# Kernel optimization log

Measured on AMD Instinct MI355X. Metric: run time of the kernel, lower is better.

## Reference

```python
import jax, jax.numpy as jnp
import numpy as np

HEADS = 16
DIM_HEAD = 64
SCALE = DIM_HEAD ** -0.5


def setup_inputs() -> dict:
    key = jax.random.key(0)
    k1, k2, k3 = jax.random.split(key, 3)
    B, N, C = 2, 2048, 1024
    inner = HEADS * DIM_HEAD  # 1024
    x = jax.random.normal(k1, (B, N, C), dtype=jnp.float32)
    w_qkv = jax.random.normal(k2, (C, 3 * inner), dtype=jnp.float32) * (C ** -0.5)
    w_proj = jax.random.normal(k3, (inner, C), dtype=jnp.float32) * (inner ** -0.5)
    b_proj = jnp.zeros((C,), dtype=jnp.float32)
    return {"x": x, "w_qkv": w_qkv, "w_proj": w_proj, "b_proj": b_proj}


def reference(x, w_qkv, w_proj, b_proj):
    B, N, C = x.shape
    qkv = x @ w_qkv  # [B, N, 3*inner]
    qkv = qkv.reshape(B, N, 3, HEADS, DIM_HEAD)
    qkv = jnp.transpose(qkv, (2, 0, 3, 1, 4))  # [3, B, H, N, D]
    q, k, v = qkv[0], qkv[1], qkv[2]
    q = q * SCALE
    attn = jnp.einsum('bhnd,bhmd->bhnm', q, k)  # [B, H, N, N]
    attn = jax.nn.softmax(attn, axis=-1)
    out = jnp.einsum('bhnm,bhmd->bhnd', attn, v)  # [B, H, N, D]
    out = jnp.transpose(out, (0, 2, 1, 3)).reshape(B, N, HEADS * DIM_HEAD)
    return out @ w_proj + b_proj
```

## Files before the change

### kernel.cpp

```cpp
#include <hip/hip_runtime.h>
#include <hip/hip_bf16.h>
#include <cstdint>
#include <cstddef>

static constexpr int BATCH = 2;
static constexpr int SEQ   = 2048;
static constexpr int CDIM  = 1024;
static constexpr int ROWS  = BATCH * SEQ;
static constexpr int QKVN  = 3 * CDIM;
static constexpr int QKN   = 2 * CDIM;

typedef short bf16x8 __attribute__((ext_vector_type(8)));
typedef short bf16x4 __attribute__((ext_vector_type(4)));
typedef float f32x4  __attribute__((ext_vector_type(4)));

__device__ inline short f2bf(float f) {
    union { float f; unsigned u; } v; v.f = f;
    unsigned u = v.u;
    u += 0x7fffu + ((u >> 16) & 1u);
    return (short)(u >> 16);
}

__device__ inline unsigned pk_bf16(float a, float b) {
#if __has_builtin(__builtin_amdgcn_cvt_pk_bf16_f32)
    auto r = __builtin_amdgcn_cvt_pk_bf16_f32(a, b);
    return __builtin_bit_cast(unsigned, r);
#else
    union { float f; unsigned u; } ua, ub;
    ua.f = a; ub.f = b;
    unsigned xa = ua.u + 0x7fffu + ((ua.u >> 16) & 1u);
    unsigned xb = ub.u + 0x7fffu + ((ub.u >> 16) & 1u);
    return __builtin_amdgcn_perm(xb, xa, 0x07060302);
#endif
}

__device__ inline void glds16(const short* g, short* l) {
    __builtin_amdgcn_global_load_lds(
        (const __attribute__((address_space(1))) void*)g,
        (__attribute__((address_space(3))) void*)l, 16, 0, 0);
}

__device__ inline f32x4 mfma16_bf16(bf16x4 a, bf16x4 b, f32x4 c) {
#if __has_builtin(__builtin_amdgcn_mfma_f32_16x16x16bf16_1k)
    return __builtin_amdgcn_mfma_f32_16x16x16bf16_1k(a, b, c, 0, 0, 0);
#else
    asm("v_mfma_f32_16x16x16_bf16 %0, %1, %2, %0" : "+v"(c) : "v"(a), "v"(b));
    return c;
#endif
}

__device__ inline int swz_src(int lane) {
    return ((lane & 3) ^ ((lane >> 3) & 3)) * 8;
}
__device__ inline int swz_rd(int quad, int l15) {
    return (quad ^ ((l15 >> 1) & 3)) * 8;
}

__global__ __launch_bounds__(256) void prep(const float* __restrict__ x,
                                            const float* __restrict__ wqkv,
                                            const float* __restrict__ wproj,
                                            short* __restrict__ x_bf,
                                            short* __restrict__ wqkvT,
                                            short* __restrict__ wprojT,
                                            float smul) {
    __shared__ float tile[32][33];
    const int bid = blockIdx.x, t = threadIdx.x;
    if (bid < 4096) {
        int i = bid * 256 + t;
        float4 f = ((const float4*)x)[i];
        uint2 o;
        o.x = pk_bf16(f.x, f.y);
        o.y = pk_bf16(f.z, f.w);
        ((uint2*)x_bf)[i] = o;
        return;
    }
    const float* in; short* out; int C, r0, c0; float scale; int srows;
    if (bid < 7168) {
        int b2 = bid - 4096;
        in = wqkv; out = wqkvT; C = QKVN;
        c0 = (b2 % 96) * 32; r0 = (b2 / 96) * 32;
        scale = smul; srows = 1024;
    } else {
        int b3 = bid - 7168;
        in = wproj; out = wprojT; C = CDIM;
        c0 = (b3 & 31) * 32; r0 = (b3 >> 5) * 32;
        scale = 1.0f; srows = 0;
    }
    int tx = t & 31, ty = t >> 5;
    #pragma unroll
    for (int i = 0; i < 4; i++)
        tile[ty + i * 8][tx] = in[(size_t)(r0 + ty + i * 8) * C + c0 + tx];
    __syncthreads();
    #pragma unroll
    for (int i = 0; i < 4; i++) {
        int orow = c0 + ty + i * 8;
        float sc = (orow < srows) ? scale : 1.0f;
        out[(size_t)orow * CDIM + r0 + tx] = f2bf(tile[tx][ty + i * 8] * sc);
    }
}

template<int BF16OUT, int MT>
__device__ __forceinline__ void gemm_core(const short* __restrict__ A,
                                          const short* __restrict__ Bt,
                                          void* __restrict__ C,
                                          const float* __restrict__ bias,
                                          int N, int K, int m0, int n0,
                                          short* As, short* Bs) {
    constexpr int AF = MT / 32;
    constexpr int APAN = MT * 32;
    constexpr int BPAN = 128 * 32;
    const int t = threadIdx.x, wave = t >> 6, lane = t & 63;
    const int l15 = lane & 15, quad = lane >> 4;
    const int wr = wave >> 1, wc = wave & 1;
    const int sg = swz_src(lane);
    const int rsl = swz_rd(quad, l15);

    f32x4 acc[AF][4] = {};

    const short* gA = A  + (size_t)(m0 + wave * (MT / 4) + (lane >> 2)) * K + sg;
    const short* gB = Bt + (size_t)(n0 + wave * 32 + (lane >> 2)) * K + sg;
    short* lA = &As[wave * (MT / 4) * 32];
    short* lB = &Bs[wave * 32 * 32];

    for (int k0 = 0; k0 < K; k0 += 64) {
        glds16(gA + k0,      lA);
        glds16(gA + k0 + 32, lA + APAN);
        if constexpr (MT == 128) {
            glds16(gA + 16 * K + k0,      lA + 512);
            glds16(gA + 16 * K + k0 + 32, lA + APAN + 512);
        }
        glds16(gB + k0,               lB);
        glds16(gB + 16 * K + k0,      lB + 512);
        glds16(gB + k0 + 32,          lB + BPAN);
        glds16(gB + 16 * K + k0 + 32, lB + BPAN + 512);
        __syncthreads();

        #pragma unroll
        for (int st = 0; st < 2; st++) {
            bf16x8 af[AF], bf[4];
            #pragma unroll
            for (int i = 0; i < AF; i++)
                af[i] = *(const bf16x8*)&As[st * APAN + (wr * (MT / 2) + i * 16 + l15) * 32 + rsl];
            #pragma unroll
            for (int j = 0; j < 4; j++)
                bf[j] = *(const bf16x8*)&Bs[st * BPAN + (wc * 64 + j * 16 + l15) * 32 + rsl];
            #pragma unroll
            for (int i = 0; i < AF; i++)
                #pragma unroll
                for (int j = 0; j < 4; j++)
                    acc[i][j] = __builtin_amdgcn_mfma_f32_16x16x32_bf16(af[i], bf[j], acc[i][j], 0, 0, 0);
        }
        __syncthreads();
    }

    #pragma unroll
    for (int i = 0; i < AF; i++) {
        #pragma unroll
        for (int j = 0; j < 4; j++) {
            #pragma unroll
            for (int r = 0; r < 4; r++) {
                int row = m0 + wr * (MT / 2) + i * 16 + quad * 4 + r;
                int col = n0 + wc * 64 + j * 16 + l15;
                float v = acc[i][j][r];
                if (BF16OUT) ((short*)C)[(size_t)row * N + col] = f2bf(v);
                else         ((float*)C)[(size_t)row * N + col] = v + bias[col];
            }
        }
    }
}

__global__ __launch_bounds__(256) void gemm_qk_v(const short* __restrict__ x_bf,
                                                 const short* __restrict__ wqkvT,
                                                 short* __restrict__ qk,
                                                 short* __restrict__ vT) {
    __shared__ __align__(16) short As[128 * 64];
    __shared__ __align__(16) short Bs[128 * 64];
    const int bid = blockIdx.x;
    if (bid < 512) {
        gemm_core<1, 128>(x_bf, wqkvT, qk, nullptr, QKN, CDIM,
                          (bid >> 4) * 128, (bid & 15) * 128, As, Bs);
    } else {
        int b2 = bid - 512;
        gemm_core<1, 128>(wqkvT + (size_t)QKN * CDIM, x_bf, vT, nullptr, ROWS, CDIM,
                          (b2 >> 5) * 128, (b2 & 31) * 128, As, Bs);
    }
}

__global__ __launch_bounds__(256) void gemm_proj(const short* __restrict__ A,
                                                 const short* __restrict__ Bt,
                                                 float* __restrict__ C,
                                                 const float* __restrict__ bias) {
    __shared__ __align__(16) short As[64 * 64];
    __shared__ __align__(16) short Bs[128 * 64];
    gemm_core<0, 64>(A, Bt, C, bias, CDIM, CDIM,
                     blockIdx.y * 64, blockIdx.x * 128, As, Bs);
}

static constexpr int KBUF  = 2 * 128 * 32;
static constexpr int VOFF  = 2 * KBUF;
static constexpr int LDV   = 136;
static constexpr int VBUF  = 64 * LDV;
static constexpr int SMEM_SH = VOFF + 2 * VBUF;

__global__ __launch_bounds__(512) void attn_kernel(const short* __restrict__ qk,
                                                   const short* __restrict__ vTg,
                                                   short* __restrict__ attn_out) {
    __shared__ __align__(16) short smem[SMEM_SH];

    const int t = threadIdx.x, wave = t >> 6, lane = t & 63;
    const int l15 = lane & 15, quad = lane >> 4;
    const int g = wave >> 2, wl = wave & 3;
    const int bh = blockIdx.y, b = bh >> 4, h = bh & 15;
    const int q0 = blockIdx.x * 128;
    const size_t baseQ = (size_t)(b * SEQ) * QKN + h * 64;
    const int rsl = swz_rd(quad, l15);

    const size_t qoff0 = baseQ + (size_t)(q0 + wl * 32 + l15) * QKN + quad * 8;
    const size_t qoff1 = qoff0 + (size_t)16 * QKN;
    bf16x8 qf00 = *(const bf16x8*)&qk[qoff0];
    bf16x8 qf01 = *(const bf16x8*)&qk[qoff0 + 32];
    bf16x8 qf10 = *(const bf16x8*)&qk[qoff1];
    bf16x8 qf11 = *(const bf16x8*)&qk[qoff1 + 32];

    const short* gK = qk + baseQ + 1024
                    + (size_t)(wave * 16 + (lane >> 2)) * QKN + swz_src(lane);
    const short* gV = vTg + (size_t)(h * 64) * ROWS + b * SEQ;
    const int vd = t >> 3, vc = t & 7;

    const bf16x4 ones = { (short)0x3F80, (short)0x3F80, (short)0x3F80, (short)0x3F80 };

    f32x4 ot0[4] = {}, ot1[4] = {};
    f32x4 ol0 = {}, ol1 = {};

    glds16(gK,      smem + wave * 512);
    glds16(gK + 32, smem + 4096 + wave * 512);
    {
        int4 va = *(const int4*)&gV[(size_t)vd * ROWS + vc * 8];
        int4 vb = *(const int4*)&gV[(size_t)vd * ROWS + 64 + vc * 8];
        *(int4*)&smem[VOFF + vd * LDV + vc * 8]      = va;
        *(int4*)&smem[VOFF + vd * LDV + 64 + vc * 8] = vb;
    }

    for (int j = 0; j < SEQ / 128; j++) {
        const int cur = j & 1, nxt = cur ^ 1;
        __syncthreads();

        int4 va, vb;
        if (j < SEQ / 128 - 1) {
            const size_t jadd = (size_t)(j + 1) * 128 * QKN;
            short* kb = smem + nxt * KBUF + wave * 512;
            glds16(gK + jadd,      kb);
            glds16(gK + jadd + 32, kb + 4096);
            va = *(const int4*)&gV[(size_t)vd * ROWS + (j + 1) * 128 + vc * 8];
            vb = *(const int4*)&gV[(size_t)vd * ROWS + (j + 1) * 128 + 64 + vc * 8];
        }

        const short* Kb0 = smem + cur * KBUF;
        const short* Kb1 = Kb0 + 4096;
        const short* Vb  = smem + VOFF + cur * VBUF;

        #pragma unroll
        for (int sub = 0; sub < 4; sub++) {
            const int gsub = g * 4 + sub;
            bf16x8 kf0 = *(const bf16x8*)&Kb0[(gsub * 16 + l15) * 32 + rsl];
            bf16x8 kf1 = *(const bf16x8*)&Kb1[(gsub * 16 + l15) * 32 + rsl];
            f32x4 a0 = {}, a1 = {};
            __builtin_amdgcn_s_setprio(1);
            a0 = __builtin_amdgcn_mfma_f32_16x16x32_bf16(kf0, qf00, a0, 0, 0, 0);
            a0 = __builtin_amdgcn_mfma_f32_16x16x32_bf16(kf1, qf01, a0, 0, 0, 0);
            a1 = __builtin_amdgcn_mfma_f32_16x16x32_bf16(kf0, qf10, a1, 0, 0, 0);
            a1 = __builtin_amdgcn_mfma_f32_16x16x32_bf16(kf1, qf11, a1, 0, 0, 0);
            __builtin_amdgcn_s_setprio(0);
            union { unsigned u[2]; bf16x4 v; } pu0, pu1;
            pu0.u[0] = pk_bf16(__builtin_amdgcn_exp2f(a0[0]), __builtin_amdgcn_exp2f(a0[1]));
            pu0.u[1] = pk_bf16(__builtin_amdgcn_exp2f(a0[2]), __builtin_amdgcn_exp2f(a0[3]));
            pu1.u[0] = pk_bf16(__builtin_amdgcn_exp2f(a1[0]), __builtin_amdgcn_exp2f(a1[1]));
            pu1.u[1] = pk_bf16(__builtin_amdgcn_exp2f(a1[2]), __builtin_amdgcn_exp2f(a1[3]));
            __builtin_amdgcn_s_setprio(1);
            ol0 = mfma16_bf16(ones, pu0.v, ol0);
            ol1 = mfma16_bf16(ones, pu1.v, ol1);
            #pragma unroll
            for (int d = 0; d < 4; d++) {
                bf16x4 vf = *(const bf16x4*)&Vb[(d * 16 + l15) * LDV + gsub * 16 + quad * 4];
                ot0[d] = mfma16_bf16(vf, pu0.v, ot0[d]);
                ot1[d] = mfma16_bf16(vf, pu1.v, ot1[d]);
            }
            __builtin_amdgcn_s_setprio(0);
        }

        if (j < SEQ / 128 - 1) {
            *(int4*)&smem[VOFF + nxt * VBUF + vd * LDV + vc * 8]      = va;
            *(int4*)&smem[VOFF + nxt * VBUF + vd * LDV + 64 + vc * 8] = vb;
        }
    }

    __syncthreads();
    float* pf   = (float*)smem;
    float* lbuf = (float*)smem + 128 * 68;
    short* tr   = smem + 18432;

    if (g == 1) {
        #pragma unroll
        for (int d = 0; d < 4; d++) {
            #pragma unroll
            for (int r = 0; r < 4; r++) {
                pf[(wl * 32 + l15) * 68      + d * 16 + quad * 4 + r] = ot0[d][r];
                pf[(wl * 32 + 16 + l15) * 68 + d * 16 + quad * 4 + r] = ot1[d][r];
            }
        }
        lbuf[wl * 32 + l15]      = ol0[0];
        lbuf[wl * 32 + 16 + l15] = ol1[0];
    }
    __syncthreads();
    if (g == 0) {
        float inv0 = 1.0f / (ol0[0] + lbuf[wl * 32 + l15]);
        float inv1 = 1.0f / (ol1[0] + lbuf[wl * 32 + 16 + l15]);
        #pragma unroll
        for (int d = 0; d < 4; d++) {
            int pb0 = (wl * 32 + l15) * 68      + d * 16 + quad * 4;
            int pb1 = (wl * 32 + 16 + l15) * 68 + d * 16 + quad * 4;
            float c00 = (ot0[d][0] + pf[pb0 + 0]) * inv0;
            float c01 = (ot0[d][1] + pf[pb0 + 1]) * inv0;
            float c02 = (ot0[d][2] + pf[pb0 + 2]) * inv0;
            float c03 = (ot0[d][3] + pf[pb0 + 3]) * inv0;
            float c10 = (ot1[d][0] + pf[pb1 + 0]) * inv1;
            float c11 = (ot1[d][1] + pf[pb1 + 1]) * inv1;
            float c12 = (ot1[d][2] + pf[pb1 + 2]) * inv1;
            float c13 = (ot1[d][3] + pf[pb1 + 3]) * inv1;
            int o0 = (wl * 32 + l15) * 72 + d * 16 + quad * 4;
            int o1 = (wl * 32 + 16 + l15) * 72 + d * 16 + quad * 4;
            *(unsigned*)&tr[o0]     = pk_bf16(c00, c01);
            *(unsigned*)&tr[o0 + 2] = pk_bf16(c02, c03);
            *(unsigned*)&tr[o1]     = pk_bf16(c10, c11);
            *(unsigned*)&tr[o1 + 2] = pk_bf16(c12, c13);
        }
    }
    __syncthreads();
    {
        int row = t >> 2, c4 = t & 3;
        #pragma unroll
        for (int p = 0; p < 2; p++) {
            int ch = c4 * 2 + p;
            int4 v = *(const int4*)&tr[row * 72 + ch * 8];
            *(int4*)&attn_out[(size_t)(b * SEQ + q0 + row) * CDIM + h * 64 + ch * 8] = v;
        }
    }
}

extern "C" void kernel_launch(void* const* d_in, const int* in_sizes, int n_in,
                              void* d_out, int out_size, void* d_ws, size_t ws_size,
                              hipStream_t stream) {
    const float* x      = (const float*)d_in[0];
    const float* w_qkv  = (const float*)d_in[1];
    const float* w_proj = (const float*)d_in[2];
    const float* b_proj = (const float*)d_in[3];
    float* out = (float*)d_out;

    char* ws = (char*)d_ws;
    short* x_bf    = (short*)(ws);
    short* wqkvT   = (short*)(ws + 8388608);
    short* wprojT  = (short*)(ws + 14680064);
    short* qk_bf   = (short*)(ws + 16777216);
    short* vTg     = (short*)(ws + 33554432);
    short* attn_bf = (short*)(ws + 41943040);

    const float SMUL = 0.125f * 1.44269504088896340736f;

    prep<<<8192, 256, 0, stream>>>(x, w_qkv, w_proj, x_bf, wqkvT, wprojT, SMUL);

    gemm_qk_v<<<768, 256, 0, stream>>>(x_bf, wqkvT, qk_bf, vTg);

    attn_kernel<<<dim3(SEQ / 128, BATCH * 16), 512, 0, stream>>>(qk_bf, vTg, attn_bf);

    gemm_proj<<<dim3(CDIM / 128, ROWS / 64), 256, 0, stream>>>(attn_bf, wprojT, out, b_proj);
}
```

Before: 184.7 us.

## Double-buffer GEMM K loop and use 128-row tiles for output projection

```diff
diff --git a/kernel.cpp b/kernel.cpp
--- a/kernel.cpp
+++ b/kernel.cpp
@@ -122,34 +122,34 @@
     short* lA = &As[wave * (MT / 4) * 32];
     short* lB = &Bs[wave * 32 * 32];
 
-    for (int k0 = 0; k0 < K; k0 += 64) {
-        glds16(gA + k0,      lA);
-        glds16(gA + k0 + 32, lA + APAN);
-        if constexpr (MT == 128) {
-            glds16(gA + 16 * K + k0,      lA + 512);
-            glds16(gA + 16 * K + k0 + 32, lA + APAN + 512);
-        }
-        glds16(gB + k0,               lB);
-        glds16(gB + 16 * K + k0,      lB + 512);
-        glds16(gB + k0 + 32,          lB + BPAN);
-        glds16(gB + 16 * K + k0 + 32, lB + BPAN + 512);
-        __syncthreads();
-
-        #pragma unroll
-        for (int st = 0; st < 2; st++) {
-            bf16x8 af[AF], bf[4];
-            #pragma unroll
-            for (int i = 0; i < AF; i++)
-                af[i] = *(const bf16x8*)&As[st * APAN + (wr * (MT / 2) + i * 16 + l15) * 32 + rsl];
+    glds16(gA, lA);
+    if constexpr (MT == 128) glds16(gA + 16 * K, lA + 512);
+    glds16(gB, lB);
+    glds16(gB + 16 * K, lB + 512);
+    __syncthreads();
+
+    const int NSTEP = K / 32;
+    for (int s = 0; s < NSTEP; s++) {
+        const int cur = s & 1, nxt = cur ^ 1;
+        if (s + 1 < NSTEP) {
+            const int k = (s + 1) * 32;
+            glds16(gA + k, lA + nxt * APAN);
+            if constexpr (MT == 128) glds16(gA + 16 * K + k, lA + nxt * APAN + 512);
+            glds16(gB + k,          lB + nxt * BPAN);
+            glds16(gB + 16 * K + k, lB + nxt * BPAN + 512);
+        }
+        bf16x8 af[AF], bfv[4];
+        #pragma unroll
+        for (int i = 0; i < AF; i++)
+            af[i] = *(const bf16x8*)&As[cur * APAN + (wr * (MT / 2) + i * 16 + l15) * 32 + rsl];
+        #pragma unroll
+        for (int j = 0; j < 4; j++)
+            bfv[j] = *(const bf16x8*)&Bs[cur * BPAN + (wc * 64 + j * 16 + l15) * 32 + rsl];
+        #pragma unroll
+        for (int i = 0; i < AF; i++)
             #pragma unroll
             for (int j = 0; j < 4; j++)
-                bf[j] = *(const bf16x8*)&Bs[st * BPAN + (wc * 64 + j * 16 + l15) * 32 + rsl];
-            #pragma unroll
-            for (int i = 0; i < AF; i++)
-                #pragma unroll
-                for (int j = 0; j < 4; j++)
-                    acc[i][j] = __builtin_amdgcn_mfma_f32_16x16x32_bf16(af[i], bf[j], acc[i][j], 0, 0, 0);
-        }
+                acc[i][j] = __builtin_amdgcn_mfma_f32_16x16x32_bf16(af[i], bfv[j], acc[i][j], 0, 0, 0);
         __syncthreads();
     }
 
@@ -173,8 +173,8 @@
                                                  const short* __restrict__ wqkvT,
                                                  short* __restrict__ qk,
                                                  short* __restrict__ vT) {
-    __shared__ __align__(16) short As[128 * 64];
-    __shared__ __align__(16) short Bs[128 * 64];
+    __shared__ __align__(16) short As[2 * 128 * 32];
+    __shared__ __align__(16) short Bs[2 * 128 * 32];
     const int bid = blockIdx.x;
     if (bid < 512) {
         gemm_core<1, 128>(x_bf, wqkvT, qk, nullptr, QKN, CDIM,
@@ -190,10 +190,10 @@
                                                  const short* __restrict__ Bt,
                                                  float* __restrict__ C,
                                                  const float* __restrict__ bias) {
-    __shared__ __align__(16) short As[64 * 64];
-    __shared__ __align__(16) short Bs[128 * 64];
-    gemm_core<0, 64>(A, Bt, C, bias, CDIM, CDIM,
-                     blockIdx.y * 64, blockIdx.x * 128, As, Bs);
+    __shared__ __align__(16) short As[2 * 128 * 32];
+    __shared__ __align__(16) short Bs[2 * 128 * 32];
+    gemm_core<0, 128>(A, Bt, C, bias, CDIM, CDIM,
+                      blockIdx.y * 128, blockIdx.x * 128, As, Bs);
 }
 
 static constexpr int KBUF  = 2 * 128 * 32;
@@ -372,5 +372,5 @@
 
     attn_kernel<<<dim3(SEQ / 128, BATCH * 16), 512, 0, stream>>>(qk_bf, vTg, attn_bf);
 
-    gemm_proj<<<dim3(CDIM / 128, ROWS / 64), 256, 0, stream>>>(attn_bf, wprojT, out, b_proj);
-}
+    gemm_proj<<<dim3(CDIM / 128, ROWS / 128), 256, 0, stream>>>(attn_bf, wprojT, out, b_proj);
+}
```

After: 196.3 us. 1.06x slower.
